# Optimization experiments

Hardware: AMD Instinct MI355X
Metric: run time of the kernel (lower is better)

The kernel has to match this reference:

```python
import jax, jax.numpy as jnp
import numpy as np

HID = 64      # hidden_size of message MLP
NF = 20       # n_node_features
EF = 20       # n_edge_features
ITERS = 3
N_ENV, N_NODES, N_EDGES = 16, 5000, 50000


def setup_inputs() -> dict:
    key = jax.random.key(0)
    ks = jax.random.split(key, 12)
    s = 0.1
    node_features = jax.random.normal(ks[0], (N_ENV, N_NODES, NF), jnp.float32)
    edges = jax.random.randint(ks[1], (2, N_EDGES), 0, N_NODES, dtype=jnp.int32)
    # msg_net: Linear(2*NF,HID) -> Tanh -> Linear(HID,HID) -> Tanh -> Linear(HID,EF)
    W1 = jax.random.normal(ks[2], (HID, 2 * NF), jnp.float32) * s
    b1 = jax.random.normal(ks[3], (HID,), jnp.float32) * s
    W2 = jax.random.normal(ks[4], (HID, HID), jnp.float32) * s
    b2 = jax.random.normal(ks[5], (HID,), jnp.float32) * s
    W3 = jax.random.normal(ks[6], (EF, HID), jnp.float32) * s
    b3 = jax.random.normal(ks[7], (EF,), jnp.float32) * s
    # GRU(input=EF, hidden=NF): weight_ih (3*NF, EF), weight_hh (3*NF, NF)
    Wih = jax.random.normal(ks[8], (3 * NF, EF), jnp.float32) * s
    Whh = jax.random.normal(ks[9], (3 * NF, NF), jnp.float32) * s
    b_ih = jax.random.normal(ks[10], (3 * NF,), jnp.float32) * s
    b_hh = jax.random.normal(ks[11], (3 * NF,), jnp.float32) * s
    return {"node_features": node_features, "edges": edges,
            "W1": W1, "b1": b1, "W2": W2, "b2": b2, "W3": W3, "b3": b3,
            "Wih": Wih, "Whh": Whh, "b_ih": b_ih, "b_hh": b_hh}


def reference(node_features, edges, W1, b1, W2, b2, W3, b3, Wih, Whh, b_ih, b_hh):
    n_env, n_nodes, _ = node_features.shape
    # Bidirectionalize edges: cat([edges, edges[[1,0]]], dim=1)
    e = jnp.concatenate([edges, edges[::-1]], axis=1)  # (2, 2E)
    src, dst = e[0], e[1]
    for _ in range(ITERS):
        # gather src/dst node feats -> message MLP
        x = jnp.concatenate([node_features[:, src], node_features[:, dst]], axis=2)  # (env, 2E, 2*NF)
        h = jnp.tanh(x @ W1.T + b1)
        h = jnp.tanh(h @ W2.T + b2)
        msg = h @ W3.T + b3  # (env, 2E, EF)
        # scatter-add messages to source nodes
        store = jnp.zeros((n_env, n_nodes, EF), node_features.dtype).at[:, src].add(msg)
        # single-step GRU update (seq_len=1, h0=node_features), vectorized over env & node
        gi = store @ Wih.T + b_ih           # (env, nodes, 3*NF)
        gh = node_features @ Whh.T + b_hh   # (env, nodes, 3*NF)
        ir, iz, in_ = jnp.split(gi, 3, axis=-1)
        hr, hz, hn = jnp.split(gh, 3, axis=-1)
        r = jax.nn.sigmoid(ir + hr)
        z = jax.nn.sigmoid(iz + hz)
        n = jnp.tanh(in_ + r * hn)
        node_features = (1.0 - z) * n + z * node_features
    return node_features
```

## Files before the change

kernel.cpp:

```cpp
#include <hip/hip_runtime.h>

#define NFEAT 20
#define EFEAT 20
#define HID   64
#define NENV  16
#define NNODES 5000
#define NEDGES 50000
#define E2 (2*NEDGES)
#define ITERS 3
#define ROWS 64
#define THREADS 128
#define NPAD 24

typedef __attribute__((ext_vector_type(8))) _Float16 f16x8;
typedef __attribute__((ext_vector_type(4))) float f32x4;

__device__ __forceinline__ ushort f2h(float f) {
    _Float16 h = (_Float16)f;
    return *(ushort*)&h;
}
__device__ __forceinline__ float fast_tanh(float x) {
    float e = __builtin_exp2f(x * 2.8853900817779268f);
    float r = __builtin_amdgcn_rcpf(e + 1.f);
    return fmaf(-2.f, r, 1.f);
}
__device__ __forceinline__ float fast_sigmoid(float x) {
    float e = __builtin_exp2f(x * -1.4426950408889634f);
    return __builtin_amdgcn_rcpf(1.f + e);
}

__global__ __launch_bounds__(256) void hist_kernel(const int* __restrict__ edges,
                                                   int* __restrict__ cnt) {
    int e = blockIdx.x * 256 + threadIdx.x;
    if (e < E2) atomicAdd(&cnt[edges[e]], 1);
}

__global__ __launch_bounds__(256) void scan_kernel(const int* __restrict__ cnt,
                                                   int* __restrict__ cursor) {
    __shared__ int part[256];
    int t = threadIdx.x;
    int local[20]; int s = 0;
    int base = t * 20;
    #pragma unroll
    for (int i = 0; i < 20; i++) {
        int idx = base + i;
        int v = (idx < NNODES) ? cnt[idx] : 0;
        local[i] = s; s += v;
    }
    part[t] = s;
    __syncthreads();
    for (int d = 1; d < 256; d <<= 1) {
        int v = (t >= d) ? part[t - d] : 0;
        __syncthreads();
        part[t] += v;
        __syncthreads();
    }
    int excl = part[t] - s;
    #pragma unroll
    for (int i = 0; i < 20; i++) {
        int idx = base + i;
        if (idx < NNODES) cursor[idx] = excl + local[i];
    }
}

__global__ __launch_bounds__(256) void scatter_kernel(const int* __restrict__ edges,
                                                      int* __restrict__ cursor,
                                                      int* __restrict__ snode,
                                                      int* __restrict__ dnode) {
    int e = blockIdx.x * 256 + threadIdx.x;
    if (e < E2) {
        int s = edges[e];
        int di = e + NEDGES; if (di >= E2) di -= E2;
        int d = edges[di];
        int pos = atomicAdd(&cursor[s], 1);
        snode[pos] = s;
        dnode[pos] = d;
    }
}

__global__ void prep_weights(const float* __restrict__ W1, const float* __restrict__ W2,
                             const float* __restrict__ W3,
                             ushort* __restrict__ W1p, ushort* __restrict__ W2p,
                             ushort* __restrict__ W3p) {
    int t = threadIdx.x;
    for (int i = t; i < 64 * 64; i += 256) {
        int n = i >> 6, k = i & 63;
        float v = 0.f;
        if (k < NFEAT)                          v = W1[n * (2 * NFEAT) + k];
        else if (k >= NPAD && k < NPAD + NFEAT) v = W1[n * (2 * NFEAT) + NFEAT + (k - NPAD)];
        W1p[i] = f2h(v);
    }
    for (int i = t; i < 64 * 64; i += 256)
        W2p[i] = f2h(W2[i]);
    for (int i = t; i < 32 * 64; i += 256) {
        int n = i >> 6, k = i & 63;
        W3p[i] = (n < EFEAT) ? f2h(W3[n * HID + k]) : (ushort)0;
    }
}

__global__ __launch_bounds__(256) void conv_nf(const float* __restrict__ nf,
                                               ushort* __restrict__ nfp) {
    int gid = blockIdx.x * 256 + threadIdx.x;
    if (gid >= NENV * NNODES) return;
    const float* p = nf + (size_t)gid * NFEAT;
    ushort* ph = nfp + (size_t)gid * NPAD;
    #pragma unroll
    for (int k = 0; k < NFEAT; k++) ph[k] = f2h(p[k]);
    *(uint2*)(ph + NFEAT) = make_uint2(0u, 0u);
}

__global__ __launch_bounds__(THREADS) void edge_mlp_mfma(
    const ushort* __restrict__ nfp,
    const int*   __restrict__ snode, const int* __restrict__ dnode,
    const ushort* __restrict__ W1p, const ushort* __restrict__ W2p,
    const ushort* __restrict__ W3p,
    const float* __restrict__ b1, const float* __restrict__ b2,
    const float* __restrict__ b3,
    float* __restrict__ store)
{
    __shared__ ushort smem16[4096];
    ushort* Hp = smem16;
    float*  msgf = (float*)smem16;
    int*    msgi = (int*)smem16;

    const int tid  = threadIdx.x;
    const int wave = tid >> 6;
    const int lane = tid & 63;
    const int lr   = lane & 15;
    const int kg   = lane >> 4;
    const int m0   = wave * 32;

#define MFMA2(acc, a0, a1, b0, b1)                                                  \
    acc = __builtin_amdgcn_mfma_f32_16x16x32_f16(a0, b0, acc, 0, 0, 0);             \
    acc = __builtin_amdgcn_mfma_f32_16x16x32_f16(a1, b1, acc, 0, 0, 0);

#define STORE_H(acc, n_)                                                            \
    {                                                                               \
        int col = (n_) * 16 + lr;                                                   \
        _Pragma("unroll")                                                           \
        for (int r = 0; r < 4; r++) {                                               \
            int row = m0 + m * 16 + kg * 4 + r;                                     \
            int idx = row * 64 + (col ^ ((row & 7) << 3));                          \
            Hp[idx] = f2h(fast_tanh(acc[r]));                                       \
        }                                                                           \
    }

    {
        f16x8 wp[4][2];
        float bb[4];
        #pragma unroll
        for (int n = 0; n < 4; n++) {
            #pragma unroll
            for (int kt = 0; kt < 2; kt++)
                wp[n][kt] = *(const f16x8*)(W1p + (n * 16 + lr) * 64 + kt * 32 + kg * 8);
            bb[n] = b1[n * 16 + lr];
        }
        #pragma unroll
        for (int m = 0; m < 2; m++) {
            int rr = m0 + m * 16 + lr;
            int gr = blockIdx.x * ROWS + rr;
            int env = gr / E2;
            int sr  = gr - env * E2;
            const ushort* sp_ = nfp + (size_t)(env * NNODES + snode[sr]) * NPAD;
            const ushort* dp_ = nfp + (size_t)(env * NNODES + dnode[sr]) * NPAD;
            f16x8 a0, a1;
            if (kg < 3) a0 = *(const f16x8*)(sp_ + kg * 8);
            else        a0 = *(const f16x8*)(dp_);
            if (kg < 2) a1 = *(const f16x8*)(dp_ + 8 + kg * 8);
            else        a1 = f16x8{(_Float16)0,(_Float16)0,(_Float16)0,(_Float16)0,
                                   (_Float16)0,(_Float16)0,(_Float16)0,(_Float16)0};
            f32x4 acc[4];
            #pragma unroll
            for (int n = 0; n < 4; n++) {
                acc[n] = f32x4{bb[n], bb[n], bb[n], bb[n]};
                MFMA2(acc[n], a0, a1, wp[n][0], wp[n][1])
            }
            #pragma unroll
            for (int n = 0; n < 4; n++) STORE_H(acc[n], n)
        }
    }

    {
        f16x8 wp[4][2];
        float bb[4];
        #pragma unroll
        for (int n = 0; n < 4; n++) {
            #pragma unroll
            for (int kt = 0; kt < 2; kt++)
                wp[n][kt] = *(const f16x8*)(W2p + (n * 16 + lr) * 64 + kt * 32 + kg * 8);
            bb[n] = b2[n * 16 + lr];
        }
        #pragma unroll
        for (int m = 0; m < 2; m++) {
            int arow = m0 + m * 16 + lr, sw = arow & 7;
            f16x8 a0 = *(const f16x8*)(Hp + arow * 64 + ((kg ^ sw) << 3));
            f16x8 a1 = *(const f16x8*)(Hp + arow * 64 + (((4 + kg) ^ sw) << 3));
            f32x4 acc[4];
            #pragma unroll
            for (int n = 0; n < 4; n++) {
                acc[n] = f32x4{bb[n], bb[n], bb[n], bb[n]};
                MFMA2(acc[n], a0, a1, wp[n][0], wp[n][1])
            }
            #pragma unroll
            for (int n = 0; n < 4; n++) STORE_H(acc[n], n)
        }
    }

    {
        int i_ = lane & 31;
        int gr_i  = blockIdx.x * ROWS + m0 + i_;
        int env_i = gr_i / E2;
        int sr_i  = gr_i - env_i * E2;
        int key   = env_i * NNODES + snode[sr_i];

        f16x8 wp[2][2];
        #pragma unroll
        for (int n = 0; n < 2; n++)
            #pragma unroll
            for (int kt = 0; kt < 2; kt++)
                wp[n][kt] = *(const f16x8*)(W3p + (n * 16 + lr) * 64 + kt * 32 + kg * 8);
        float bb0 = b3[lr];
        float bb1 = (lr < 4) ? b3[16 + lr] : 0.f;

        f32x4 acc0[2], acc1[2];
        #pragma unroll
        for (int m = 0; m < 2; m++) {
            int arow = m0 + m * 16 + lr, sw = arow & 7;
            f16x8 a0 = *(const f16x8*)(Hp + arow * 64 + ((kg ^ sw) << 3));
            f16x8 a1 = *(const f16x8*)(Hp + arow * 64 + (((4 + kg) ^ sw) << 3));
            acc0[m] = f32x4{bb0, bb0, bb0, bb0};
            acc1[m] = f32x4{bb1, bb1, bb1, bb1};
            MFMA2(acc0[m], a0, a1, wp[0][0], wp[0][1])
            MFMA2(acc1[m], a0, a1, wp[1][0], wp[1][1])
        }

        int wbase = wave * 1024;
        #pragma unroll
        for (int m = 0; m < 2; m++) {
            #pragma unroll
            for (int r = 0; r < 4; r++) {
                int lrow = m * 16 + kg * 4 + r;
                msgf[wbase + lrow * 25 + lr] = acc0[m][r];
                if (lr < 4) msgf[wbase + lrow * 25 + 16 + lr] = acc1[m][r];
            }
        }
        if (lane < 32) msgi[wbase + lane * 25 + 24] = key;

        int nxt = __shfl_down(key, 1);
        bool flag = (i_ == 31) || (key != nxt);
        unsigned fm = (unsigned)__ballot(flag);

        if (lane < EFEAT) {
            int c = lane;
            float sum = 0.f;
            for (int i = 0; i < 32; i++) {
                sum += msgf[wbase + i * 25 + c];
                if ((fm >> i) & 1u) {
                    int curk = msgi[wbase + i * 25 + 24];
                    atomicAdd(store + (size_t)curk * EFEAT + c, sum);
                    sum = 0.f;
                }
            }
        }
    }
#undef STORE_H
#undef MFMA2
}

__global__ __launch_bounds__(256) void gru_kernel(
    const float* __restrict__ store,
    const float* __restrict__ Wih, const float* __restrict__ bih,
    const float* __restrict__ Whh, const float* __restrict__ bhh,
    float* __restrict__ nf,
    ushort* __restrict__ nfp)
{
    int gid = blockIdx.x * blockDim.x + threadIdx.x;
    const int total = NENV * NNODES;
    if (gid >= total) return;

    const float* s = store + (size_t)gid * EFEAT;
    float*       h = nf    + (size_t)gid * NFEAT;
    ushort*     ph = nfp   + (size_t)gid * NPAD;

    float sv[EFEAT], hv[NFEAT];
    #pragma unroll
    for (int k = 0; k < EFEAT; k++) sv[k] = s[k];
    #pragma unroll
    for (int k = 0; k < NFEAT; k++) hv[k] = h[k];

    for (int t = 0; t < NFEAT; t++) {
        float ir = bih[t],            hr = bhh[t];
        float iz = bih[NFEAT + t],    hz = bhh[NFEAT + t];
        float in_ = bih[2*NFEAT + t], hn = bhh[2*NFEAT + t];
        const float* wr = Wih + t * EFEAT;
        const float* wz = Wih + (NFEAT + t) * EFEAT;
        const float* wn = Wih + (2*NFEAT + t) * EFEAT;
        #pragma unroll
        for (int k = 0; k < EFEAT; k++) {
            ir  = fmaf(sv[k], wr[k], ir);
            iz  = fmaf(sv[k], wz[k], iz);
            in_ = fmaf(sv[k], wn[k], in_);
        }
        const float* vr = Whh + t * NFEAT;
        const float* vz = Whh + (NFEAT + t) * NFEAT;
        const float* vn = Whh + (2*NFEAT + t) * NFEAT;
        #pragma unroll
        for (int k = 0; k < NFEAT; k++) {
            hr = fmaf(hv[k], vr[k], hr);
            hz = fmaf(hv[k], vz[k], hz);
            hn = fmaf(hv[k], vn[k], hn);
        }
        float r = fast_sigmoid(ir + hr);
        float z = fast_sigmoid(iz + hz);
        float n = fast_tanh(in_ + r * hn);
        float hw = (1.f - z) * n + z * hv[t];
        h[t] = hw;
        ph[t] = f2h(hw);
    }
    *(uint2*)(ph + NFEAT) = make_uint2(0u, 0u);
}

extern "C" void kernel_launch(void* const* d_in, const int* in_sizes, int n_in,
                              void* d_out, int out_size, void* d_ws, size_t ws_size,
                              hipStream_t stream) {
    const float* nf_in = (const float*)d_in[0];
    const int*   edges = (const int*)d_in[1];
    const float* W1 = (const float*)d_in[2];
    const float* b1 = (const float*)d_in[3];
    const float* W2 = (const float*)d_in[4];
    const float* b2 = (const float*)d_in[5];
    const float* W3 = (const float*)d_in[6];
    const float* b3 = (const float*)d_in[7];
    const float* Wih = (const float*)d_in[8];
    const float* Whh = (const float*)d_in[9];
    const float* bih = (const float*)d_in[10];
    const float* bhh = (const float*)d_in[11];

    float* nf    = (float*)d_out;
    float* store = (float*)d_ws;
    const size_t nf_bytes    = (size_t)NENV * NNODES * NFEAT * sizeof(float);
    const size_t store_bytes = (size_t)NENV * NNODES * EFEAT * sizeof(float);
    ushort* W1p = (ushort*)((char*)d_ws + store_bytes);
    ushort* W2p = W1p + 64 * 64;
    ushort* W3p = W2p + 64 * 64;
    ushort* nfp = W3p + 32 * 64;
    int* cnt    = (int*)(nfp + (size_t)NENV * NNODES * NPAD);
    int* cursor = cnt + NNODES;
    int* snode  = cursor + NNODES;
    int* dnode  = snode + E2;

    prep_weights<<<1, 256, 0, stream>>>(W1, W2, W3, W1p, W2p, W3p);
    conv_nf<<<(NENV * NNODES + 255) / 256, 256, 0, stream>>>(nf_in, nfp);
    hipMemcpyAsync(nf, nf_in, nf_bytes, hipMemcpyDeviceToDevice, stream);
    hipMemsetAsync(cnt, 0, NNODES * sizeof(int), stream);
    hist_kernel<<<(E2 + 255) / 256, 256, 0, stream>>>(edges, cnt);
    scan_kernel<<<1, 256, 0, stream>>>(cnt, cursor);
    scatter_kernel<<<(E2 + 255) / 256, 256, 0, stream>>>(edges, cursor, snode, dnode);

    const int edge_blocks = (NENV * E2) / ROWS;
    dim3 grid_n((NENV * NNODES + 255) / 256);

    for (int it = 0; it < ITERS; it++) {
        hipMemsetAsync(store, 0, store_bytes, stream);
        edge_mlp_mfma<<<edge_blocks, THREADS, 0, stream>>>(nfp, snode, dnode,
                                                           W1p, W2p, W3p,
                                                           b1, b2, b3, store);
        gru_kernel<<<grid_n, 256, 0, stream>>>(store, Wih, bih, Whh, bhh, nf, nfp);
    }
}
```

Baseline: 565.3 us.

## Transpose MFMA operands so outputs are row-contiguous, use packed LDS stores

Swaps the A/B operand roles in the message MLP MFMAs so each lane's accumulator holds four consecutive hidden features of one edge row instead of four rows of one feature. This allows tanh results to be packed into half2 pairs and written to shared memory as single 8-byte stores, and biases to load as vectors. The message staging buffer moves from a stride-25 layout to a stride-32 XOR-swizzled layout with 16-byte vector stores. The aim is fewer scalar LDS writes and conversions, in exchange for more intricate swizzle indexing.

```diff
diff --git a/kernel.cpp b/kernel.cpp
--- a/kernel.cpp
+++ b/kernel.cpp
@@ -13,11 +13,16 @@
 #define NPAD 24
 
 typedef __attribute__((ext_vector_type(8))) _Float16 f16x8;
+typedef __attribute__((ext_vector_type(2))) __fp16  h16x2;
 typedef __attribute__((ext_vector_type(4))) float f32x4;
 
 __device__ __forceinline__ ushort f2h(float f) {
     _Float16 h = (_Float16)f;
     return *(ushort*)&h;
+}
+__device__ __forceinline__ unsigned pk2h(float a, float b) {
+    h16x2 p = __builtin_amdgcn_cvt_pkrtz(a, b);
+    return *(unsigned*)&p;
 }
 __device__ __forceinline__ float fast_tanh(float x) {
     float e = __builtin_exp2f(x * 2.8853900817779268f);
@@ -130,79 +135,78 @@
     const int kg   = lane >> 4;
     const int m0   = wave * 32;
 
-#define MFMA2(acc, a0, a1, b0, b1)                                                  \
-    acc = __builtin_amdgcn_mfma_f32_16x16x32_f16(a0, b0, acc, 0, 0, 0);             \
-    acc = __builtin_amdgcn_mfma_f32_16x16x32_f16(a1, b1, acc, 0, 0, 0);
-
-#define STORE_H(acc, n_)                                                            \
+#define MFMA2(acc, w0, w1, x0, x1)                                                  \
+    acc = __builtin_amdgcn_mfma_f32_16x16x32_f16(w0, x0, acc, 0, 0, 0);             \
+    acc = __builtin_amdgcn_mfma_f32_16x16x32_f16(w1, x1, acc, 0, 0, 0);
+
+#define STORE_H4(accv, m_, rr_)                                                     \
     {                                                                               \
-        int col = (n_) * 16 + lr;                                                   \
-        _Pragma("unroll")                                                           \
-        for (int r = 0; r < 4; r++) {                                               \
-            int row = m0 + m * 16 + kg * 4 + r;                                     \
-            int idx = row * 64 + (col ^ ((row & 7) << 3));                          \
-            Hp[idx] = f2h(fast_tanh(acc[r]));                                       \
-        }                                                                           \
+        float t0 = fast_tanh(accv[0]), t1 = fast_tanh(accv[1]);                     \
+        float t2 = fast_tanh(accv[2]), t3 = fast_tanh(accv[3]);                     \
+        unsigned p01 = pk2h(t0, t1), p23 = pk2h(t2, t3);                            \
+        int c8 = (m_) * 2 + (kg >> 1);                                              \
+        int idx = (rr_) * 64 + ((c8 ^ ((rr_) & 7)) << 3) + ((kg & 1) << 2);         \
+        *(uint2*)(Hp + idx) = make_uint2(p01, p23);                                 \
     }
 
     {
         f16x8 wp[4][2];
-        float bb[4];
-        #pragma unroll
-        for (int n = 0; n < 4; n++) {
+        f32x4 bb[4];
+        #pragma unroll
+        for (int m = 0; m < 4; m++) {
             #pragma unroll
             for (int kt = 0; kt < 2; kt++)
-                wp[n][kt] = *(const f16x8*)(W1p + (n * 16 + lr) * 64 + kt * 32 + kg * 8);
-            bb[n] = b1[n * 16 + lr];
-        }
-        #pragma unroll
-        for (int m = 0; m < 2; m++) {
-            int rr = m0 + m * 16 + lr;
+                wp[m][kt] = *(const f16x8*)(W1p + (m * 16 + lr) * 64 + kt * 32 + kg * 8);
+            bb[m] = *(const f32x4*)(b1 + m * 16 + kg * 4);
+        }
+        #pragma unroll
+        for (int n = 0; n < 2; n++) {
+            int rr = m0 + n * 16 + lr;
             int gr = blockIdx.x * ROWS + rr;
             int env = gr / E2;
             int sr  = gr - env * E2;
             const ushort* sp_ = nfp + (size_t)(env * NNODES + snode[sr]) * NPAD;
             const ushort* dp_ = nfp + (size_t)(env * NNODES + dnode[sr]) * NPAD;
-            f16x8 a0, a1;
-            if (kg < 3) a0 = *(const f16x8*)(sp_ + kg * 8);
-            else        a0 = *(const f16x8*)(dp_);
-            if (kg < 2) a1 = *(const f16x8*)(dp_ + 8 + kg * 8);
-            else        a1 = f16x8{(_Float16)0,(_Float16)0,(_Float16)0,(_Float16)0,
+            f16x8 x0, x1;
+            if (kg < 3) x0 = *(const f16x8*)(sp_ + kg * 8);
+            else        x0 = *(const f16x8*)(dp_);
+            if (kg < 2) x1 = *(const f16x8*)(dp_ + 8 + kg * 8);
+            else        x1 = f16x8{(_Float16)0,(_Float16)0,(_Float16)0,(_Float16)0,
                                    (_Float16)0,(_Float16)0,(_Float16)0,(_Float16)0};
             f32x4 acc[4];
             #pragma unroll
-            for (int n = 0; n < 4; n++) {
-                acc[n] = f32x4{bb[n], bb[n], bb[n], bb[n]};
-                MFMA2(acc[n], a0, a1, wp[n][0], wp[n][1])
+            for (int m = 0; m < 4; m++) {
+                acc[m] = bb[m];
+                MFMA2(acc[m], wp[m][0], wp[m][1], x0, x1)
             }
             #pragma unroll
-            for (int n = 0; n < 4; n++) STORE_H(acc[n], n)
+            for (int m = 0; m < 4; m++) STORE_H4(acc[m], m, rr)
         }
     }
 
     {
         f16x8 wp[4][2];
-        float bb[4];
-        #pragma unroll
-        for (int n = 0; n < 4; n++) {
+        f32x4 bb[4];
+        #pragma unroll
+        for (int m = 0; m < 4; m++) {
             #pragma unroll
             for (int kt = 0; kt < 2; kt++)
-                wp[n][kt] = *(const f16x8*)(W2p + (n * 16 + lr) * 64 + kt * 32 + kg * 8);
-            bb[n] = b2[n * 16 + lr];
-        }
-        #pragma unroll
-        for (int m = 0; m < 2; m++) {
-            int arow = m0 + m * 16 + lr, sw = arow & 7;
-            f16x8 a0 = *(const f16x8*)(Hp + arow * 64 + ((kg ^ sw) << 3));
-            f16x8 a1 = *(const f16x8*)(Hp + arow * 64 + (((4 + kg) ^ sw) << 3));
+                wp[m][kt] = *(const f16x8*)(W2p + (m * 16 + lr) * 64 + kt * 32 + kg * 8);
+            bb[m] = *(const f32x4*)(b2 + m * 16 + kg * 4);
+        }
+        #pragma unroll
+        for (int n = 0; n < 2; n++) {
+            int rr = m0 + n * 16 + lr, sw = rr & 7;
+            f16x8 x0 = *(const f16x8*)(Hp + rr * 64 + ((kg ^ sw) << 3));
+            f16x8 x1 = *(const f16x8*)(Hp + rr * 64 + (((4 + kg) ^ sw) << 3));
             f32x4 acc[4];
             #pragma unroll
-            for (int n = 0; n < 4; n++) {
-                acc[n] = f32x4{bb[n], bb[n], bb[n], bb[n]};
-                MFMA2(acc[n], a0, a1, wp[n][0], wp[n][1])
+            for (int m = 0; m < 4; m++) {
+                acc[m] = bb[m];
+                MFMA2(acc[m], wp[m][0], wp[m][1], x0, x1)
             }
             #pragma unroll
-            for (int n = 0; n < 4; n++) STORE_H(acc[n], n)
+            for (int m = 0; m < 4; m++) STORE_H4(acc[m], m, rr)
         }
     }
 
@@ -213,57 +217,63 @@
         int sr_i  = gr_i - env_i * E2;
         int key   = env_i * NNODES + snode[sr_i];
 
-        f16x8 wp[2][2];
-        #pragma unroll
-        for (int n = 0; n < 2; n++)
+        f16x8 w3[2][2];
+        #pragma unroll
+        for (int m = 0; m < 2; m++)
             #pragma unroll
             for (int kt = 0; kt < 2; kt++)
-                wp[n][kt] = *(const f16x8*)(W3p + (n * 16 + lr) * 64 + kt * 32 + kg * 8);
-        float bb0 = b3[lr];
-        float bb1 = (lr < 4) ? b3[16 + lr] : 0.f;
-
+                w3[m][kt] = *(const f16x8*)(W3p + (m * 16 + lr) * 64 + kt * 32 + kg * 8);
+        f32x4 bb0 = *(const f32x4*)(b3 + kg * 4);
+        f32x4 bb1 = (kg == 0) ? *(const f32x4*)(b3 + 16)
+                              : f32x4{0.f, 0.f, 0.f, 0.f};
+
+        f16x8 xb[2][2];
+        #pragma unroll
+        for (int n = 0; n < 2; n++) {
+            int rr = m0 + n * 16 + lr, sw = rr & 7;
+            xb[n][0] = *(const f16x8*)(Hp + rr * 64 + ((kg ^ sw) << 3));
+            xb[n][1] = *(const f16x8*)(Hp + rr * 64 + (((4 + kg) ^ sw) << 3));
+        }
         f32x4 acc0[2], acc1[2];
         #pragma unroll
-        for (int m = 0; m < 2; m++) {
-            int arow = m0 + m * 16 + lr, sw = arow & 7;
-            f16x8 a0 = *(const f16x8*)(Hp + arow * 64 + ((kg ^ sw) << 3));
-            f16x8 a1 = *(const f16x8*)(Hp + arow * 64 + (((4 + kg) ^ sw) << 3));
-            acc0[m] = f32x4{bb0, bb0, bb0, bb0};
-            acc1[m] = f32x4{bb1, bb1, bb1, bb1};
-            MFMA2(acc0[m], a0, a1, wp[0][0], wp[0][1])
-            MFMA2(acc1[m], a0, a1, wp[1][0], wp[1][1])
+        for (int n = 0; n < 2; n++) {
+            acc0[n] = bb0;
+            MFMA2(acc0[n], w3[0][0], w3[0][1], xb[n][0], xb[n][1])
+            acc1[n] = bb1;
+            MFMA2(acc1[n], w3[1][0], w3[1][1], xb[n][0], xb[n][1])
         }
 
         int wbase = wave * 1024;
         #pragma unroll
-        for (int m = 0; m < 2; m++) {
-            #pragma unroll
-            for (int r = 0; r < 4; r++) {
-                int lrow = m * 16 + kg * 4 + r;
-                msgf[wbase + lrow * 25 + lr] = acc0[m][r];
-                if (lr < 4) msgf[wbase + lrow * 25 + 16 + lr] = acc1[m][r];
+        for (int n = 0; n < 2; n++) {
+            int row = n * 16 + lr;
+            int g0 = kg ^ (row & 7);
+            *(f32x4*)(msgf + wbase + row * 32 + (g0 << 2)) = acc0[n];
+            if (kg == 0) {
+                int g1 = 4 ^ (row & 7);
+                *(f32x4*)(msgf + wbase + row * 32 + (g1 << 2)) = acc1[n];
             }
         }
-        if (lane < 32) msgi[wbase + lane * 25 + 24] = key;
+        if (lane < 32) msgi[wbase + i_ * 32 + ((5 ^ (i_ & 7)) << 2)] = key;
 
         int nxt = __shfl_down(key, 1);
         bool flag = (i_ == 31) || (key != nxt);
         unsigned fm = (unsigned)__ballot(flag);
 
         if (lane < EFEAT) {
-            int c = lane;
+            int c = lane, g = c >> 2, o = c & 3;
             float sum = 0.f;
             for (int i = 0; i < 32; i++) {
-                sum += msgf[wbase + i * 25 + c];
+                sum += msgf[wbase + i * 32 + ((g ^ (i & 7)) << 2) + o];
                 if ((fm >> i) & 1u) {
-                    int curk = msgi[wbase + i * 25 + 24];
+                    int curk = msgi[wbase + i * 32 + ((5 ^ (i & 7)) << 2)];
                     atomicAdd(store + (size_t)curk * EFEAT + c, sum);
                     sum = 0.f;
                 }
             }
         }
     }
-#undef STORE_H
+#undef STORE_H4
 #undef MFMA2
 }
 
```

New measurement: 567.4 us. Within noise of the previous version (+0.4%).
